# Performance work log

Measured on AMD Instinct MI355X. Metric: run time of the kernel, lower is better.

Reference implementation:

```python
import jax, jax.numpy as jnp
import numpy as np

N = 2_000_000   # num_instances
F = 64          # feature_dim
S = 65536       # number of multisets (max_index)


def setup_inputs() -> dict:
    key = jax.random.key(0)
    k1, k2, k3, k4 = jax.random.split(key, 4)
    x = jax.random.normal(k1, (N, F), dtype=jnp.float32)
    batch_idx = jax.random.randint(k2, (N,), 0, S, dtype=jnp.int64)
    # learned params: convex weight t ~ U(0,1) per feature, xavier-normal linear weight [1, 5]
    t = jax.random.uniform(k3, (F,), dtype=jnp.float32)
    num_coords = 5  # add_sum=True -> [n, min, max, relu_sum, sum]
    xavier_std = np.sqrt(2.0 / (num_coords + 1))
    W = jax.random.normal(k4, (1, num_coords), dtype=jnp.float32) * xavier_std
    return {"x": x, "batch_idx": batch_idx, "max_index": S, "t": t, "W": W}


def reference(x, batch_idx, max_index, t, W):
    # clamp_convex_weight=True: t is clamped to [0, 1]
    t = jnp.clip(t, 0.0, 1.0)
    # per-segment multi-stat reduction: min, max, sum, count  -> [S, F]
    mn = jax.ops.segment_min(x, batch_idx, num_segments=max_index)
    mx = jax.ops.segment_max(x, batch_idx, num_segments=max_index)
    sums = jax.ops.segment_sum(x, batch_idx, num_segments=max_index)
    counts = jax.ops.segment_sum(jnp.ones((x.shape[0],), dtype=x.dtype), batch_idx,
                                 num_segments=max_index)  # [S]
    # gather min/max back to instances, adaptive bias, relu, scatter-sum
    bias = t * mx[batch_idx] + (1.0 - t) * mn[batch_idx]          # [N, F]
    relu_sum = jax.ops.segment_sum(jax.nn.relu(x - bias), batch_idx,
                                   num_segments=max_index)         # [S, F]
    n = jnp.broadcast_to(counts[:, None], mn.shape)                # [S, F]
    # cat along -1 then reshape [S,5,F].permute(0,2,1) == stack stats on last axis
    coords = jnp.stack([n, mn, mx, relu_sum, sums], axis=-1)       # [S, F, 5]
    out = jnp.einsum('sfc,oc->sfo', coords, W)[..., 0]             # [S, F]
    return out
```

## Files before the change

### kernel.cpp

```cpp
#include <hip/hip_runtime.h>
#include <math.h>

#define NSEG 65536
#define FDIM 64
#define CAP  56

__global__ __launch_bounds__(256) void hist_kernel(const int* __restrict__ idx,
                                                   int* __restrict__ counts, int n) {
    int i = blockIdx.x * blockDim.x + threadIdx.x;
    int stride = gridDim.x * blockDim.x;
    for (; i < n; i += stride)
        atomicAdd(&counts[idx[i]], 1);
}

__global__ __launch_bounds__(1024) void scan_kernel(const int* __restrict__ counts,
                                                    int* __restrict__ offs,
                                                    int* __restrict__ cursor) {
    __shared__ int part[1024];
    const int tid  = threadIdx.x;
    const int base = tid * 64;
    int s = 0;
    for (int j = 0; j < 64; ++j) s += counts[base + j];
    part[tid] = s;
    __syncthreads();
    for (int off = 1; off < 1024; off <<= 1) {
        int v = (tid >= off) ? part[tid - off] : 0;
        __syncthreads();
        part[tid] += v;
        __syncthreads();
    }
    int run = part[tid] - s;
    for (int j = 0; j < 64; ++j) {
        offs[base + j]   = run;
        cursor[base + j] = run;
        run += counts[base + j];
    }
}

__global__ __launch_bounds__(256) void scatter_kernel(const int* __restrict__ idx,
                                                      int* __restrict__ cursor,
                                                      int* __restrict__ sorted, int n) {
    int i = blockIdx.x * blockDim.x + threadIdx.x;
    int stride = gridDim.x * blockDim.x;
    for (; i < n; i += stride) {
        int s = idx[i];
        int p = atomicAdd(&cursor[s], 1);
        sorted[p] = i;
    }
}

__global__ __launch_bounds__(256) void seg_main(const float* __restrict__ x,
                                                const int* __restrict__ sorted,
                                                const int* __restrict__ offs,
                                                const int* __restrict__ cursor,
                                                const float* __restrict__ t,
                                                const float* __restrict__ W,
                                                float* __restrict__ out) {
    const int s    = blockIdx.x;
    const int lane = threadIdx.x & 63;
    const int w    = threadIdx.x >> 6;
    const int beg  = offs[s];
    const int cnt  = cursor[s] - beg;

    __shared__ float rows[CAP][FDIM];
    __shared__ float cmn[4][FDIM];
    __shared__ float cmx[4][FDIM];
    __shared__ float csm[4][FDIM];

    const int per = (cnt + 3) >> 2;
    const int r0  = min(cnt, w * per);
    const int r1  = min(cnt, r0 + per);

    float mn = INFINITY, mx = -INFINITY, sm = 0.0f;

    int r = r0;
    for (; r + 4 <= r1; r += 4) {
        int q0 = sorted[beg + r + 0];
        int q1 = sorted[beg + r + 1];
        int q2 = sorted[beg + r + 2];
        int q3 = sorted[beg + r + 3];
        float v0 = x[(size_t)q0 * FDIM + lane];
        float v1 = x[(size_t)q1 * FDIM + lane];
        float v2 = x[(size_t)q2 * FDIM + lane];
        float v3 = x[(size_t)q3 * FDIM + lane];
        if (r + 0 < CAP) rows[r + 0][lane] = v0;
        if (r + 1 < CAP) rows[r + 1][lane] = v1;
        if (r + 2 < CAP) rows[r + 2][lane] = v2;
        if (r + 3 < CAP) rows[r + 3][lane] = v3;
        mn = fminf(mn, fminf(fminf(v0, v1), fminf(v2, v3)));
        mx = fmaxf(mx, fmaxf(fmaxf(v0, v1), fmaxf(v2, v3)));
        sm += (v0 + v1) + (v2 + v3);
    }
    for (; r < r1; ++r) {
        int q = sorted[beg + r];
        float v = x[(size_t)q * FDIM + lane];
        if (r < CAP) rows[r][lane] = v;
        mn = fminf(mn, v);
        mx = fmaxf(mx, v);
        sm += v;
    }

    cmn[w][lane] = mn; cmx[w][lane] = mx; csm[w][lane] = sm;
    __syncthreads();
    mn = fminf(fminf(cmn[0][lane], cmn[1][lane]), fminf(cmn[2][lane], cmn[3][lane]));
    mx = fmaxf(fmaxf(cmx[0][lane], cmx[1][lane]), fmaxf(cmx[2][lane], cmx[3][lane]));
    const float smT = (csm[0][lane] + csm[1][lane]) + (csm[2][lane] + csm[3][lane]);
    __syncthreads();

    const float tc   = fminf(fmaxf(t[lane], 0.0f), 1.0f);
    const float bias = tc * mx + (1.0f - tc) * mn;
    float rs = 0.0f;
    const int lim = min(r1, CAP);
    for (r = r0; r < lim; ++r)
        rs += fmaxf(0.0f, rows[r][lane] - bias);
    for (r = max(r0, CAP); r < r1; ++r) {
        int q = sorted[beg + r];
        rs += fmaxf(0.0f, x[(size_t)q * FDIM + lane] - bias);
    }
    cmn[w][lane] = rs;
    __syncthreads();

    if (w == 0) {
        const float rsT = (cmn[0][lane] + cmn[1][lane]) + (cmn[2][lane] + cmn[3][lane]);
        out[(size_t)s * FDIM + lane] =
            W[0] * (float)cnt + W[1] * mn + W[2] * mx + W[3] * rsT + W[4] * smT;
    }
}

extern "C" void kernel_launch(void* const* d_in, const int* in_sizes, int n_in,
                              void* d_out, int out_size, void* d_ws, size_t ws_size,
                              hipStream_t stream) {
    const float* x    = (const float*)d_in[0];
    const int*   bidx = (const int*)d_in[1];
    const float* t    = (const float*)d_in[3];
    const float* W    = (const float*)d_in[4];
    float*       out  = (float*)d_out;
    const int    N    = in_sizes[0] / FDIM;

    int* counts = (int*)d_ws;
    int* offs   = counts + NSEG;
    int* cursor = offs + NSEG;
    int* sorted = cursor + NSEG;

    hipMemsetAsync(counts, 0, NSEG * sizeof(int), stream);

    hist_kernel<<<2048, 256, 0, stream>>>(bidx, counts, N);
    scan_kernel<<<1, 1024, 0, stream>>>(counts, offs, cursor);
    scatter_kernel<<<2048, 256, 0, stream>>>(bidx, cursor, sorted, N);
    seg_main<<<NSEG, 256, 0, stream>>>(x, sorted, offs, cursor, t, W, out);
}
```

Before: 1.020 ms.

## Vectorize index loads, split scan into three-phase multi-block, deepen gather unroll

The histogram and scatter kernels now read indices as int4, and the single-block 1024-thread scan becomes a three-kernel multi-block scan (block sums, scan of block sums, local scan with base). The main segment kernel unrolls row gathers to 8 with nontemporal loads, removes one barrier by giving the relu sums their own shared array, and writes the output with a nontemporal store. Together these aim to cut scan latency, index-read overhead and gather latency. The int4 paths assume N is divisible by 4, and the scan adds two extra kernel launches.

```diff
diff --git a/kernel.cpp b/kernel.cpp
--- a/kernel.cpp
+++ b/kernel.cpp
@@ -6,46 +6,82 @@
 #define CAP  56
 
 __global__ __launch_bounds__(256) void hist_kernel(const int* __restrict__ idx,
-                                                   int* __restrict__ counts, int n) {
+                                                   int* __restrict__ counts, int n4) {
+    const int4* v = (const int4*)idx;
     int i = blockIdx.x * blockDim.x + threadIdx.x;
     int stride = gridDim.x * blockDim.x;
-    for (; i < n; i += stride)
-        atomicAdd(&counts[idx[i]], 1);
+    for (; i < n4; i += stride) {
+        int4 a = v[i];
+        atomicAdd(&counts[a.x], 1);
+        atomicAdd(&counts[a.y], 1);
+        atomicAdd(&counts[a.z], 1);
+        atomicAdd(&counts[a.w], 1);
+    }
 }
 
-__global__ __launch_bounds__(1024) void scan_kernel(const int* __restrict__ counts,
-                                                    int* __restrict__ offs,
-                                                    int* __restrict__ cursor) {
-    __shared__ int part[1024];
-    const int tid  = threadIdx.x;
-    const int base = tid * 64;
-    int s = 0;
-    for (int j = 0; j < 64; ++j) s += counts[base + j];
-    part[tid] = s;
+__global__ __launch_bounds__(256) void scan1(const int* __restrict__ counts,
+                                             int* __restrict__ bsum) {
+    __shared__ int red[256];
+    int t = threadIdx.x;
+    red[t] = counts[blockIdx.x * 256 + t];
     __syncthreads();
-    for (int off = 1; off < 1024; off <<= 1) {
-        int v = (tid >= off) ? part[tid - off] : 0;
-        __syncthreads();
-        part[tid] += v;
+    for (int off = 128; off > 0; off >>= 1) {
+        if (t < off) red[t] += red[t + off];
         __syncthreads();
     }
-    int run = part[tid] - s;
-    for (int j = 0; j < 64; ++j) {
-        offs[base + j]   = run;
-        cursor[base + j] = run;
-        run += counts[base + j];
+    if (t == 0) bsum[blockIdx.x] = red[0];
+}
+
+__global__ __launch_bounds__(256) void scan2(const int* __restrict__ bsum,
+                                             int* __restrict__ bbase) {
+    __shared__ int p[256];
+    int t = threadIdx.x;
+    int v = bsum[t];
+    p[t] = v;
+    __syncthreads();
+    for (int off = 1; off < 256; off <<= 1) {
+        int u = (t >= off) ? p[t - off] : 0;
+        __syncthreads();
+        p[t] += u;
+        __syncthreads();
     }
+    bbase[t] = p[t] - v;
+}
+
+__global__ __launch_bounds__(256) void scan3(const int* __restrict__ counts,
+                                             const int* __restrict__ bbase,
+                                             int* __restrict__ offs,
+                                             int* __restrict__ cursor) {
+    __shared__ int p[256];
+    int t = threadIdx.x;
+    int g = blockIdx.x * 256 + t;
+    int v = counts[g];
+    p[t] = v;
+    __syncthreads();
+    for (int off = 1; off < 256; off <<= 1) {
+        int u = (t >= off) ? p[t - off] : 0;
+        __syncthreads();
+        p[t] += u;
+        __syncthreads();
+    }
+    int e = bbase[blockIdx.x] + p[t] - v;
+    offs[g]   = e;
+    cursor[g] = e;
 }
 
 __global__ __launch_bounds__(256) void scatter_kernel(const int* __restrict__ idx,
                                                       int* __restrict__ cursor,
-                                                      int* __restrict__ sorted, int n) {
+                                                      int* __restrict__ sorted, int n4) {
+    const int4* v = (const int4*)idx;
     int i = blockIdx.x * blockDim.x + threadIdx.x;
     int stride = gridDim.x * blockDim.x;
-    for (; i < n; i += stride) {
-        int s = idx[i];
-        int p = atomicAdd(&cursor[s], 1);
-        sorted[p] = i;
+    for (; i < n4; i += stride) {
+        int4 a = v[i];
+        int b = i * 4;
+        int p0 = atomicAdd(&cursor[a.x], 1); sorted[p0] = b + 0;
+        int p1 = atomicAdd(&cursor[a.y], 1); sorted[p1] = b + 1;
+        int p2 = atomicAdd(&cursor[a.z], 1); sorted[p2] = b + 2;
+        int p3 = atomicAdd(&cursor[a.w], 1); sorted[p3] = b + 3;
     }
 }
 
@@ -63,9 +99,7 @@
     const int cnt  = cursor[s] - beg;
 
     __shared__ float rows[CAP][FDIM];
-    __shared__ float cmn[4][FDIM];
-    __shared__ float cmx[4][FDIM];
-    __shared__ float csm[4][FDIM];
+    __shared__ float cmn[4][FDIM], cmx[4][FDIM], csm[4][FDIM], crs[4][FDIM];
 
     const int per = (cnt + 3) >> 2;
     const int r0  = min(cnt, w * per);
@@ -74,30 +108,31 @@
     float mn = INFINITY, mx = -INFINITY, sm = 0.0f;
 
     int r = r0;
-    for (; r + 4 <= r1; r += 4) {
-        int q0 = sorted[beg + r + 0];
-        int q1 = sorted[beg + r + 1];
-        int q2 = sorted[beg + r + 2];
-        int q3 = sorted[beg + r + 3];
-        float v0 = x[(size_t)q0 * FDIM + lane];
-        float v1 = x[(size_t)q1 * FDIM + lane];
-        float v2 = x[(size_t)q2 * FDIM + lane];
-        float v3 = x[(size_t)q3 * FDIM + lane];
-        if (r + 0 < CAP) rows[r + 0][lane] = v0;
-        if (r + 1 < CAP) rows[r + 1][lane] = v1;
-        if (r + 2 < CAP) rows[r + 2][lane] = v2;
-        if (r + 3 < CAP) rows[r + 3][lane] = v3;
-        mn = fminf(mn, fminf(fminf(v0, v1), fminf(v2, v3)));
-        mx = fmaxf(mx, fmaxf(fmaxf(v0, v1), fmaxf(v2, v3)));
-        sm += (v0 + v1) + (v2 + v3);
+    for (; r + 8 <= r1; r += 8) {
+        int q[8];
+#pragma unroll
+        for (int k = 0; k < 8; ++k) q[k] = sorted[beg + r + k];
+        float v[8];
+#pragma unroll
+        for (int k = 0; k < 8; ++k)
+            v[k] = __builtin_nontemporal_load(&x[(size_t)q[k] * FDIM + lane]);
+#pragma unroll
+        for (int k = 0; k < 8; ++k)
+            if (r + k < CAP) rows[r + k][lane] = v[k];
+#pragma unroll
+        for (int k = 0; k < 8; ++k) {
+            mn = fminf(mn, v[k]);
+            mx = fmaxf(mx, v[k]);
+        }
+        sm += ((v[0] + v[1]) + (v[2] + v[3])) + ((v[4] + v[5]) + (v[6] + v[7]));
     }
     for (; r < r1; ++r) {
         int q = sorted[beg + r];
-        float v = x[(size_t)q * FDIM + lane];
-        if (r < CAP) rows[r][lane] = v;
-        mn = fminf(mn, v);
-        mx = fmaxf(mx, v);
-        sm += v;
+        float vv = __builtin_nontemporal_load(&x[(size_t)q * FDIM + lane]);
+        if (r < CAP) rows[r][lane] = vv;
+        mn = fminf(mn, vv);
+        mx = fmaxf(mx, vv);
+        sm += vv;
     }
 
     cmn[w][lane] = mn; cmx[w][lane] = mx; csm[w][lane] = sm;
@@ -105,7 +140,6 @@
     mn = fminf(fminf(cmn[0][lane], cmn[1][lane]), fminf(cmn[2][lane], cmn[3][lane]));
     mx = fmaxf(fmaxf(cmx[0][lane], cmx[1][lane]), fmaxf(cmx[2][lane], cmx[3][lane]));
     const float smT = (csm[0][lane] + csm[1][lane]) + (csm[2][lane] + csm[3][lane]);
-    __syncthreads();
 
     const float tc   = fminf(fmaxf(t[lane], 0.0f), 1.0f);
     const float bias = tc * mx + (1.0f - tc) * mn;
@@ -117,13 +151,13 @@
         int q = sorted[beg + r];
         rs += fmaxf(0.0f, x[(size_t)q * FDIM + lane] - bias);
     }
-    cmn[w][lane] = rs;
+    crs[w][lane] = rs;
     __syncthreads();
 
     if (w == 0) {
-        const float rsT = (cmn[0][lane] + cmn[1][lane]) + (cmn[2][lane] + cmn[3][lane]);
-        out[(size_t)s * FDIM + lane] =
-            W[0] * (float)cnt + W[1] * mn + W[2] * mx + W[3] * rsT + W[4] * smT;
+        const float rsT = (crs[0][lane] + crs[1][lane]) + (crs[2][lane] + crs[3][lane]);
+        float o = W[0] * (float)cnt + W[1] * mn + W[2] * mx + W[3] * rsT + W[4] * smT;
+        __builtin_nontemporal_store(o, &out[(size_t)s * FDIM + lane]);
     }
 }
 
@@ -136,16 +170,21 @@
     const float* W    = (const float*)d_in[4];
     float*       out  = (float*)d_out;
     const int    N    = in_sizes[0] / FDIM;
+    const int    N4   = N >> 2;
 
     int* counts = (int*)d_ws;
     int* offs   = counts + NSEG;
     int* cursor = offs + NSEG;
-    int* sorted = cursor + NSEG;
+    int* bsum   = cursor + NSEG;
+    int* bbase  = bsum + 256;
+    int* sorted = bbase + 256;
 
     hipMemsetAsync(counts, 0, NSEG * sizeof(int), stream);
 
-    hist_kernel<<<2048, 256, 0, stream>>>(bidx, counts, N);
-    scan_kernel<<<1, 1024, 0, stream>>>(counts, offs, cursor);
-    scatter_kernel<<<2048, 256, 0, stream>>>(bidx, cursor, sorted, N);
+    hist_kernel<<<1024, 256, 0, stream>>>(bidx, counts, N4);
+    scan1<<<256, 256, 0, stream>>>(counts, bsum);
+    scan2<<<1, 256, 0, stream>>>(bsum, bbase);
+    scan3<<<256, 256, 0, stream>>>(counts, bbase, offs, cursor);
+    scatter_kernel<<<1024, 256, 0, stream>>>(bidx, cursor, sorted, N4);
     seg_main<<<NSEG, 256, 0, stream>>>(x, sorted, offs, cursor, t, W, out);
 }
```

Measured after the change: 989.5 us. 1.03x faster.
